# Kernel tuning notes

Hardware: AMD Instinct MI355X
Metric: run time of the kernel (lower is better)

The kernel has to match this reference:

```python
import jax, jax.numpy as jnp
import numpy as np
from jax import lax

DIM = 384
HEADS = 8
DIM_HEAD = 64
INNER = HEADS * DIM_HEAD  # 512
K = 3
B, H, W = 8, 56, 56
EPS = 1e-5
SCALE = DIM_HEAD ** -0.5


def _dw_proj(x, w_dw, bn_g, bn_b, bn_m, bn_v, w_pw):
    """DepthWiseConv2d: depthwise kxk conv (groups=C_in) -> BatchNorm (inference) -> 1x1 conv."""
    c_in = x.shape[1]
    y = lax.conv_general_dilated(
        x, w_dw, window_strides=(1, 1), padding='SAME',
        feature_group_count=c_in,
        dimension_numbers=('NCHW', 'OIHW', 'NCHW'))
    inv = bn_g / jnp.sqrt(bn_v + EPS)
    y = y * inv[None, :, None, None] + (bn_b - bn_m * inv)[None, :, None, None]
    # 1x1 conv as einsum over channels
    return jnp.einsum('bchw,oc->bohw', y, w_pw)


def _split_heads(t):
    # b (h d) x y -> (b h) (x y) d
    b, _, hh, ww = t.shape
    t = t.reshape(b, HEADS, DIM_HEAD, hh * ww)
    return t.transpose(0, 1, 3, 2).reshape(b * HEADS, hh * ww, DIM_HEAD)


def setup_inputs() -> dict:
    key = jax.random.key(0)
    ks = jax.random.split(key, 12)
    inp = {
        'x': jax.random.normal(ks[0], (B, DIM, H, W), jnp.float32),
        'wq_dw': jax.random.normal(ks[1], (DIM, 1, K, K), jnp.float32) * 0.1,
        'wq_bn_g': jax.random.normal(ks[2], (DIM,), jnp.float32) * 0.1 + 1.0,
        'wq_bn_b': jax.random.normal(ks[3], (DIM,), jnp.float32) * 0.1,
        'wq_bn_m': jax.random.normal(ks[4], (DIM,), jnp.float32) * 0.1,
        'wq_bn_v': jax.random.uniform(ks[5], (DIM,), jnp.float32, 0.5, 1.5),
        'wq_pw': jax.random.normal(ks[6], (INNER, DIM), jnp.float32) * (DIM ** -0.5),
        'wkv_dw': jax.random.normal(ks[7], (DIM, 1, K, K), jnp.float32) * 0.1,
        'wkv_bn_g': jax.random.normal(ks[8], (DIM,), jnp.float32) * 0.1 + 1.0,
        'wkv_bn_b': jax.random.normal(ks[9], (DIM,), jnp.float32) * 0.1,
        'wkv_bn_m': jax.random.normal(ks[10], (DIM,), jnp.float32) * 0.1,
        'wkv_bn_v': jax.random.uniform(ks[11], (DIM,), jnp.float32, 0.5, 1.5),
    }
    k2 = jax.random.split(jax.random.fold_in(key, 1), 3)
    inp['wkv_pw'] = jax.random.normal(k2[0], (2 * INNER, DIM), jnp.float32) * (DIM ** -0.5)
    inp['wo'] = jax.random.normal(k2[1], (DIM, INNER), jnp.float32) * (INNER ** -0.5)
    inp['bo'] = jax.random.normal(k2[2], (DIM,), jnp.float32) * 0.01
    return inp


def reference(x, wq_dw, wq_bn_g, wq_bn_b, wq_bn_m, wq_bn_v, wq_pw,
              wkv_dw, wkv_bn_g, wkv_bn_b, wkv_bn_m, wkv_bn_v, wkv_pw, wo, bo):
    b, _, hh, ww = x.shape
    q = _dw_proj(x, wq_dw, wq_bn_g, wq_bn_b, wq_bn_m, wq_bn_v, wq_pw)
    kv = _dw_proj(x, wkv_dw, wkv_bn_g, wkv_bn_b, wkv_bn_m, wkv_bn_v, wkv_pw)
    k, v = kv[:, :INNER], kv[:, INNER:]
    q, k, v = _split_heads(q), _split_heads(k), _split_heads(v)  # (b*h, N, d)

    # Original math: M0 = diag((q*k).sum(-1))*s; M1+M2 = s*q@k^T;
    # out = M0.sum()*v + (M1 - M0)@v + M2@v = M0.sum()*v + s*q@(k^T@v) - diag*v
    diag = (q * k).sum(-1) * SCALE              # (bh, N)
    m0_sum = diag.sum()                          # global scalar
    ktv = jnp.einsum('bnd,bne->bde', k, v)       # (bh, d, d) -- O(N d^2)
    out = m0_sum * v + SCALE * jnp.einsum('bnd,bde->bne', q, ktv) - diag[..., None] * v

    # (b h) (x y) d -> b (h d) x y
    out = out.reshape(b, HEADS, hh * ww, DIM_HEAD).transpose(0, 1, 3, 2)
    out = out.reshape(b, INNER, hh, ww)
    # to_out: 1x1 conv with bias (dropout p=0)
    return jnp.einsum('bchw,oc->bohw', out, wo) + bo[None, :, None, None]
```

## Files before the change

kernel.cpp:

```cpp
#include <hip/hip_runtime.h>

typedef unsigned short u16;

#define N_SP   3136
#define BNCOL  25088
#define NDIM   384
#define NINNER 512
#define SCALE_F 0.125f

typedef __attribute__((ext_vector_type(8))) short bf16x8;
typedef __attribute__((ext_vector_type(4))) float f32x4;

#define AS1 __attribute__((address_space(1)))
#define AS3 __attribute__((address_space(3)))

__device__ __forceinline__ float bf2f(u16 u) {
  union { unsigned int i; float f; } v; v.i = ((unsigned int)u) << 16; return v.f;
}
__device__ __forceinline__ u16 f2bf(float f) {
  union { float f; unsigned int i; } v; v.f = f;
  unsigned int r = v.i + 0x7fffu + ((v.i >> 16) & 1u);
  return (u16)(r >> 16);
}

__device__ __forceinline__ void g2l16(const u16* g, u16* l) {
  __builtin_amdgcn_global_load_lds((const AS1 unsigned int*)g,
                                   (AS3 unsigned int*)l, 16, 0, 0);
}

__global__ __launch_bounds__(256) void cvt_kernel(
    const float* __restrict__ a, const float* __restrict__ b, const float* __restrict__ c,
    u16* __restrict__ oa, u16* __restrict__ ob, u16* __restrict__ oc,
    const float* __restrict__ qdw, const float* __restrict__ qg, const float* __restrict__ qb2,
    const float* __restrict__ qm,  const float* __restrict__ qv,
    const float* __restrict__ kdw, const float* __restrict__ kg, const float* __restrict__ kb2,
    const float* __restrict__ km,  const float* __restrict__ kvv,
    float* __restrict__ fused)
{
  int i = blockIdx.x * 256 + threadIdx.x;
  if (i < 196608) oa[i] = f2bf(a[i]);
  ob[i] = f2bf(b[i]);
  if (i < 196608) oc[i] = f2bf(c[i]);
  if (i < NDIM) {
    float invq = qg[i] * rsqrtf(qv[i] + 1e-5f);
    float invk = kg[i] * rsqrtf(kvv[i] + 1e-5f);
    float* f = fused + i * 20;
#pragma unroll
    for (int j = 0; j < 9; ++j) { f[j] = qdw[i*9+j] * invq; f[10+j] = kdw[i*9+j] * invk; }
    f[9]  = qb2[i] - qm[i] * invq;
    f[19] = kb2[i] - km[i] * invk;
  }
}

__global__ __launch_bounds__(256) void dwbn_kernel(
    const float* __restrict__ x, const float* __restrict__ fused,
    u16* __restrict__ yq, u16* __restrict__ ykv)
{
  __shared__ u16 Lq[64][40];
  __shared__ u16 Lk[64][40];
  int tid = threadIdx.x;
  int bb = blockIdx.z, c0 = blockIdx.y * 32, p0 = blockIdx.x * 64;
  int pl = tid & 63;
  int cg = __builtin_amdgcn_readfirstlane(tid >> 6);
  int p = p0 + pl;
  int h = p / 56, w = p - h * 56;
  int roff[3], coff[3];
  float mr[3], mc[3];
#pragma unroll
  for (int d = 0; d < 3; ++d) {
    int r = h + d - 1;
    bool vr = (r >= 0) && (r < 56);
    roff[d] = (vr ? r : h) * 56;
    mr[d] = vr ? 1.f : 0.f;
    int cc = w + d - 1;
    bool vc = (cc >= 0) && (cc < 56);
    coff[d] = vc ? cc : w;
    mc[d] = vc ? 1.f : 0.f;
  }
  float m9[9];
#pragma unroll
  for (int dh = 0; dh < 3; ++dh)
#pragma unroll
    for (int dw = 0; dw < 3; ++dw) m9[dh*3+dw] = mr[dh] * mc[dw];

  __attribute__((aligned(16))) u16 oq[8], ok[8];
#pragma unroll
  for (int i = 0; i < 8; ++i) {
    int c = c0 + cg * 8 + i;
    const float* xp = x + ((size_t)bb * NDIM + c) * N_SP;
    const float* f = fused + c * 20;
    float v[9];
#pragma unroll
    for (int dh = 0; dh < 3; ++dh)
#pragma unroll
      for (int dw = 0; dw < 3; ++dw)
        v[dh*3+dw] = xp[roff[dh] + coff[dw]];
    float sq = f[9], sk = f[19];
#pragma unroll
    for (int j = 0; j < 9; ++j) {
      float xm = v[j] * m9[j];
      sq += xm * f[j];
      sk += xm * f[10+j];
    }
    oq[i] = f2bf(sq); ok[i] = f2bf(sk);
  }
  *(ushort4*)&Lq[pl][cg * 8]     = *(ushort4*)&oq[0];
  *(ushort4*)&Lq[pl][cg * 8 + 4] = *(ushort4*)&oq[4];
  *(ushort4*)&Lk[pl][cg * 8]     = *(ushort4*)&ok[0];
  *(ushort4*)&Lk[pl][cg * 8 + 4] = *(ushort4*)&ok[4];
  __syncthreads();
  int pr = tid >> 2, cc2 = (tid & 3) * 8;
  size_t g = ((size_t)bb * N_SP + p0 + pr) * NDIM + c0 + cc2;
  *(ushort4*)(yq + g)      = *(ushort4*)&Lq[pr][cc2];
  *(ushort4*)(yq + g + 4)  = *(ushort4*)&Lq[pr][cc2 + 4];
  *(ushort4*)(ykv + g)     = *(ushort4*)&Lk[pr][cc2];
  *(ushort4*)(ykv + g + 4) = *(ushort4*)&Lk[pr][cc2 + 4];
}

__global__ __launch_bounds__(256) void mfma_gemm(
    const u16* __restrict__ A, const u16* __restrict__ B, int Kd,
    u16* __restrict__ Cout, int Cstride,
    int mode, const float* __restrict__ bias, float* __restrict__ Out, int Mt, int Nt)
{
  __shared__ union {
    struct { u16 A[128 * 32]; u16 B[128 * 32]; } s;
    u16 T[64 * 132];
  } lds;
  int bid = blockIdx.x, mt, nt;
  if (Nt == 8) { nt = bid & 7; mt = bid >> 3; }
  else {
    int r = bid & 7, g = bid >> 3;
    mt = g % Mt; nt = (g / Mt) * 8 + r;
    if (nt >= Nt) return;
  }
  int m0 = mt * 128, n0 = nt * 128;

  int tid = threadIdx.x;
  int lane = tid & 63, wv = tid >> 6;
  int wm = (wv >> 1) * 64, wn = (wv & 1) * 64;
  int srow = lane >> 2;
  int sch = (lane & 3) * 8;
  int arow0 = wv * 32;
  const u16* Ag = A + (size_t)(m0 + arow0 + srow) * Kd + sch;
  const u16* Bg = B + (size_t)(n0 + arow0 + srow) * Kd + sch;
  u16* Al = &lds.s.A[arow0 * 32];
  u16* Bl = &lds.s.B[arow0 * 32];
  f32x4 acc[4][4];
#pragma unroll
  for (int i = 0; i < 4; ++i)
#pragma unroll
    for (int j = 0; j < 4; ++j) acc[i][j] = (f32x4){0.f, 0.f, 0.f, 0.f};

  int ml = lane & 15, q8 = (lane >> 4) * 8;
  for (int k0 = 0; k0 < Kd; k0 += 32) {
    g2l16(Ag + k0, Al);
    g2l16(Ag + k0 + (size_t)16 * Kd, Al + 16 * 32);
    g2l16(Bg + k0, Bl);
    g2l16(Bg + k0 + (size_t)16 * Kd, Bl + 16 * 32);
    __syncthreads();
    bf16x8 af[4], bfr[4];
#pragma unroll
    for (int i = 0; i < 4; ++i) {
      af[i]  = *(const bf16x8*)&lds.s.A[(wm + i * 16 + ml) * 32 + q8];
      bfr[i] = *(const bf16x8*)&lds.s.B[(wn + i * 16 + ml) * 32 + q8];
    }
#pragma unroll
    for (int i = 0; i < 4; ++i)
#pragma unroll
      for (int j = 0; j < 4; ++j)
        acc[i][j] = __builtin_amdgcn_mfma_f32_16x16x32_bf16(af[i], bfr[j], acc[i][j], 0, 0, 0);
    __syncthreads();
  }

  if (mode == 0) {
    int q4 = (lane >> 4) * 4;
#pragma unroll
    for (int ph = 0; ph < 2; ++ph) {
      if (ph) __syncthreads();
      if ((wv & 1) == ph) {
#pragma unroll
        for (int i = 0; i < 4; ++i)
#pragma unroll
          for (int j = 0; j < 4; ++j) {
            int nl = j * 16 + ml;
            int m = wm + i * 16 + q4;
            ushort4 o;
            o.x = f2bf(acc[i][j][0]); o.y = f2bf(acc[i][j][1]);
            o.z = f2bf(acc[i][j][2]); o.w = f2bf(acc[i][j][3]);
            *(ushort4*)&lds.T[nl * 132 + m] = o;
          }
      }
      __syncthreads();
#pragma unroll
      for (int it = 0; it < 4; ++it) {
        int nl = it * 16 + (tid >> 4);
        int mc = (tid & 15) * 8;
        ushort4 a = *(ushort4*)&lds.T[nl * 132 + mc];
        ushort4 b = *(ushort4*)&lds.T[nl * 132 + mc + 4];
        u16* gp = Cout + (size_t)(n0 + ph * 64 + nl) * Cstride + m0 + mc;
        *(ushort4*)gp = a;
        *(ushort4*)(gp + 4) = b;
      }
    }
  } else {
    int q4 = (lane >> 4) * 4;
#pragma unroll
    for (int i = 0; i < 4; ++i)
#pragma unroll
      for (int j = 0; j < 4; ++j) {
        int n = n0 + wn + j * 16 + ml;
        int bb = n / N_SP, p = n - bb * N_SP;
#pragma unroll
        for (int rr = 0; rr < 4; ++rr) {
          int m = m0 + wm + i * 16 + q4 + rr;
          Out[((size_t)bb * NDIM + m) * N_SP + p] = acc[i][j][rr] + bias[m];
        }
      }
  }
}

__global__ __launch_bounds__(256) void diag_kernel(
    const u16* __restrict__ Q, const u16* __restrict__ KV,
    float* __restrict__ dg, float* __restrict__ m0)
{
  int hh = blockIdx.y;
  int bn = blockIdx.x * 256 + threadIdx.x;
  const u16* qrow = Q + (size_t)bn * NINNER + hh * 64;
  const u16* kcol = KV + (size_t)(hh * 64) * BNCOL + bn;
  float s = 0.f;
#pragma unroll
  for (int d0 = 0; d0 < 64; d0 += 8) {
    ushort4 a = *(const ushort4*)(qrow + d0);
    ushort4 b = *(const ushort4*)(qrow + d0 + 4);
    const u16* kp = kcol + (size_t)d0 * BNCOL;
    s += bf2f(a.x) * bf2f(kp[0]);
    s += bf2f(a.y) * bf2f(kp[(size_t)1 * BNCOL]);
    s += bf2f(a.z) * bf2f(kp[(size_t)2 * BNCOL]);
    s += bf2f(a.w) * bf2f(kp[(size_t)3 * BNCOL]);
    s += bf2f(b.x) * bf2f(kp[(size_t)4 * BNCOL]);
    s += bf2f(b.y) * bf2f(kp[(size_t)5 * BNCOL]);
    s += bf2f(b.z) * bf2f(kp[(size_t)6 * BNCOL]);
    s += bf2f(b.w) * bf2f(kp[(size_t)7 * BNCOL]);
  }
  s *= SCALE_F;
  dg[(size_t)bn * 8 + hh] = s;
  float r = s;
#pragma unroll
  for (int off = 32; off > 0; off >>= 1) r += __shfl_down(r, off);
  __shared__ float wsum[4];
  if ((threadIdx.x & 63) == 0) wsum[threadIdx.x >> 6] = r;
  __syncthreads();
  if (threadIdx.x == 0) atomicAdd(m0, wsum[0] + wsum[1] + wsum[2] + wsum[3]);
}

__global__ __launch_bounds__(256) void ktv_kernel(
    const u16* __restrict__ KV, float* __restrict__ ktv)
{
  int bh = blockIdx.y, bb = bh >> 3, hh = bh & 7;
  int tid = threadIdx.x;
  int w = tid >> 6, lane = tid & 63;
  int ml = lane & 15, quad = lane >> 4, q8 = quad * 8;
  size_t colbase = (size_t)bb * N_SP + blockIdx.x * 224 + q8;
  const u16* Ar = KV + (size_t)(hh * 64 + w * 16 + ml) * BNCOL + colbase;
  const u16* Br = KV + (size_t)(NINNER + hh * 64 + ml) * BNCOL + colbase;
  f32x4 acc[4];
#pragma unroll
  for (int j = 0; j < 4; ++j) acc[j] = (f32x4){0.f, 0.f, 0.f, 0.f};
#pragma unroll
  for (int t = 0; t < 7; ++t) {
    int po = t * 32;
    bf16x8 a = *(const bf16x8*)(Ar + po);
#pragma unroll
    for (int j = 0; j < 4; ++j) {
      bf16x8 b = *(const bf16x8*)(Br + (size_t)j * 16 * BNCOL + po);
      acc[j] = __builtin_amdgcn_mfma_f32_16x16x32_bf16(a, b, acc[j], 0, 0, 0);
    }
  }
  float* kt = ktv + bh * 4096;
#pragma unroll
  for (int j = 0; j < 4; ++j)
#pragma unroll
    for (int r = 0; r < 4; ++r)
      atomicAdd(&kt[(w * 16 + quad * 4 + r) * 64 + j * 16 + ml], acc[j][r]);
}

__global__ __launch_bounds__(256) void attn_out_kernel(
    const u16* __restrict__ Q, const u16* __restrict__ KV,
    const float* __restrict__ dg, const float* __restrict__ ktv,
    const float* __restrict__ m0p, u16* __restrict__ OutA)
{
  __shared__ u16 Bt[64][72];
  __shared__ u16 T2[64][72];
  __shared__ float ds2[64];
  int bh = blockIdx.y, bb = bh >> 3, hh = bh & 7;
  int p0 = blockIdx.x * 64;
  int tid = threadIdx.x;
  const float* kt = ktv + bh * 4096;
  for (int l = tid; l < 4096; l += 256) {
    int d = l >> 6, e = l & 63;
    Bt[e][d] = f2bf(kt[l]);
  }
  if (tid < 64) ds2[tid] = dg[(size_t)(bb * N_SP + p0 + tid) * 8 + hh];
  __syncthreads();
  int w = tid >> 6, lane = tid & 63;
  int ml = lane & 15, quad = lane >> 4, q8 = quad * 8;
  const u16* Ar = Q + ((size_t)bb * N_SP + p0 + w * 16 + ml) * NINNER + hh * 64 + q8;
  bf16x8 a0 = *(const bf16x8*)Ar;
  bf16x8 a1 = *(const bf16x8*)(Ar + 32);
  f32x4 acc[4];
#pragma unroll
  for (int j = 0; j < 4; ++j) acc[j] = (f32x4){0.f, 0.f, 0.f, 0.f};
#pragma unroll
  for (int j = 0; j < 4; ++j) {
    bf16x8 b0 = *(const bf16x8*)&Bt[j * 16 + ml][q8];
    bf16x8 b1 = *(const bf16x8*)&Bt[j * 16 + ml][32 + q8];
    acc[j] = __builtin_amdgcn_mfma_f32_16x16x32_bf16(a0, b0, acc[j], 0, 0, 0);
    acc[j] = __builtin_amdgcn_mfma_f32_16x16x32_bf16(a1, b1, acc[j], 0, 0, 0);
  }
  float m0v = *m0p;
  size_t pcol = (size_t)bb * N_SP + p0 + w * 16 + quad * 4;
#pragma unroll
  for (int j = 0; j < 4; ++j) {
    const u16* vr = KV + (size_t)(NINNER + hh * 64 + j * 16 + ml) * BNCOL + pcol;
    ushort4 vv = *(const ushort4*)vr;
    const u16* vp = (const u16*)&vv;
#pragma unroll
    for (int r = 0; r < 4; ++r) {
      float dvm = m0v - ds2[w * 16 + quad * 4 + r];
      float o = SCALE_F * acc[j][r] + dvm * bf2f(vp[r]);
      T2[w * 16 + quad * 4 + r][j * 16 + ml] = f2bf(o);
    }
  }
  __syncthreads();
  int pl = tid >> 2, ec = (tid & 3) * 16;
  u16* gp = OutA + ((size_t)bb * N_SP + p0 + pl) * NINNER + hh * 64 + ec;
  *(ushort4*)gp        = *(ushort4*)&T2[pl][ec];
  *(ushort4*)(gp + 4)  = *(ushort4*)&T2[pl][ec + 4];
  *(ushort4*)(gp + 8)  = *(ushort4*)&T2[pl][ec + 8];
  *(ushort4*)(gp + 12) = *(ushort4*)&T2[pl][ec + 12];
}

extern "C" void kernel_launch(void* const* d_in, const int* in_sizes, int n_in,
                              void* d_out, int out_size, void* d_ws, size_t ws_size,
                              hipStream_t stream)
{
  (void)in_sizes; (void)n_in; (void)out_size; (void)ws_size;
  const float* x      = (const float*)d_in[0];
  const float* wq_dw  = (const float*)d_in[1];
  const float* wq_g   = (const float*)d_in[2];
  const float* wq_b   = (const float*)d_in[3];
  const float* wq_m   = (const float*)d_in[4];
  const float* wq_v   = (const float*)d_in[5];
  const float* wq_pw  = (const float*)d_in[6];
  const float* wkv_dw = (const float*)d_in[7];
  const float* wkv_g  = (const float*)d_in[8];
  const float* wkv_b  = (const float*)d_in[9];
  const float* wkv_m  = (const float*)d_in[10];
  const float* wkv_v  = (const float*)d_in[11];
  const float* wkv_pw = (const float*)d_in[12];
  const float* wo     = (const float*)d_in[13];
  const float* bo     = (const float*)d_in[14];
  float* out = (float*)d_out;

  char* ws = (char*)d_ws;
  size_t off = 0;
  auto alloc = [&](size_t bytes) {
    void* p = ws + off; off = (off + bytes + 255) & ~(size_t)255; return p;
  };
  u16* yq   = (u16*)alloc((size_t)BNCOL * NDIM * 2);
  u16* ykv  = (u16*)alloc((size_t)BNCOL * NDIM * 2);
  u16* Qb   = (u16*)alloc((size_t)BNCOL * NINNER * 2);
  u16* KVb  = (u16*)alloc((size_t)2 * NINNER * BNCOL * 2);
  float* dgb  = (float*)alloc((size_t)BNCOL * 8 * 4);
  float* ktvb = (float*)alloc((size_t)64 * 4096 * 4 + 64);
  u16* Wq  = (u16*)alloc((size_t)NINNER * NDIM * 2);
  u16* Wkv = (u16*)alloc((size_t)2 * NINNER * NDIM * 2);
  u16* Wo  = (u16*)alloc((size_t)NDIM * NINNER * 2);
  float* fused = (float*)alloc((size_t)NDIM * 20 * 4);
  float* m0 = ktvb + 64 * 4096;
  u16* OutA = yq;

  hipMemsetAsync(ktvb, 0, (size_t)64 * 4096 * 4 + 4, stream);

  cvt_kernel<<<1536, 256, 0, stream>>>(wq_pw, wkv_pw, wo, Wq, Wkv, Wo,
                                       wq_dw, wq_g, wq_b, wq_m, wq_v,
                                       wkv_dw, wkv_g, wkv_b, wkv_m, wkv_v, fused);

  dwbn_kernel<<<dim3(49, 12, 8), 256, 0, stream>>>(x, fused, yq, ykv);

  mfma_gemm<<<dim3(4 * 200), 256, 0, stream>>>(Wq, yq, NDIM, Qb, NINNER, 0, nullptr, nullptr, 4, 196);
  mfma_gemm<<<dim3(196 * 8), 256, 0, stream>>>(ykv, Wkv, NDIM, KVb, BNCOL, 0, nullptr, nullptr, 196, 8);

  diag_kernel<<<dim3(98, 8), 256, 0, stream>>>(Qb, KVb, dgb, m0);
  ktv_kernel<<<dim3(14, 64), 256, 0, stream>>>(KVb, ktvb);
  attn_out_kernel<<<dim3(49, 64), 256, 0, stream>>>(Qb, KVb, dgb, ktvb, m0, OutA);

  mfma_gemm<<<dim3(3 * 200), 256, 0, stream>>>(Wo, OutA, NINNER, nullptr, 0, 1, bo, out, 3, 196);
}
```

Before: 296.9 us.

## Merge Q and KV projections into one GEMM with channel-major QKV layout

Interleaves the depthwise outputs into a single 768-wide activation buffer and concatenates the Q and KV pointwise weights, so one GEMM launch computes Q, K and V. All three are stored channel-major (d x BNCOL) and written straight from registers, dropping the LDS transpose epilogue. The diag, ktv and attention-output kernels are adapted to the new layout, with K^T V stored transposed and Q gathered with strided loads. The goal is fewer launches and better wave fill. The costs are uncoalesced 2-byte scattered stores in the GEMM epilogue and strided scalar Q loads in attn_out.

```diff
diff --git a/kernel.cpp b/kernel.cpp
--- a/kernel.cpp
+++ b/kernel.cpp
@@ -30,7 +30,7 @@
 
 __global__ __launch_bounds__(256) void cvt_kernel(
     const float* __restrict__ a, const float* __restrict__ b, const float* __restrict__ c,
-    u16* __restrict__ oa, u16* __restrict__ ob, u16* __restrict__ oc,
+    u16* __restrict__ wqkv, u16* __restrict__ wo_o,
     const float* __restrict__ qdw, const float* __restrict__ qg, const float* __restrict__ qb2,
     const float* __restrict__ qm,  const float* __restrict__ qv,
     const float* __restrict__ kdw, const float* __restrict__ kg, const float* __restrict__ kb2,
@@ -38,9 +38,9 @@
     float* __restrict__ fused)
 {
   int i = blockIdx.x * 256 + threadIdx.x;
-  if (i < 196608) oa[i] = f2bf(a[i]);
-  ob[i] = f2bf(b[i]);
-  if (i < 196608) oc[i] = f2bf(c[i]);
+  if (i < 196608) wqkv[i] = f2bf(a[i]);
+  wqkv[196608 + i] = f2bf(b[i]);
+  if (i < 196608) wo_o[i] = f2bf(c[i]);
   if (i < NDIM) {
     float invq = qg[i] * rsqrtf(qv[i] + 1e-5f);
     float invk = kg[i] * rsqrtf(kvv[i] + 1e-5f);
@@ -54,7 +54,7 @@
 
 __global__ __launch_bounds__(256) void dwbn_kernel(
     const float* __restrict__ x, const float* __restrict__ fused,
-    u16* __restrict__ yq, u16* __restrict__ ykv)
+    u16* __restrict__ yact)
 {
   __shared__ u16 Lq[64][40];
   __shared__ u16 Lk[64][40];
@@ -110,30 +110,27 @@
   *(ushort4*)&Lk[pl][cg * 8 + 4] = *(ushort4*)&ok[4];
   __syncthreads();
   int pr = tid >> 2, cc2 = (tid & 3) * 8;
-  size_t g = ((size_t)bb * N_SP + p0 + pr) * NDIM + c0 + cc2;
-  *(ushort4*)(yq + g)      = *(ushort4*)&Lq[pr][cc2];
-  *(ushort4*)(yq + g + 4)  = *(ushort4*)&Lq[pr][cc2 + 4];
-  *(ushort4*)(ykv + g)     = *(ushort4*)&Lk[pr][cc2];
-  *(ushort4*)(ykv + g + 4) = *(ushort4*)&Lk[pr][cc2 + 4];
+  size_t g = ((size_t)bb * N_SP + p0 + pr) * 768 + c0 + cc2;
+  *(ushort4*)(yact + g)            = *(ushort4*)&Lq[pr][cc2];
+  *(ushort4*)(yact + g + 4)        = *(ushort4*)&Lq[pr][cc2 + 4];
+  *(ushort4*)(yact + g + 384)      = *(ushort4*)&Lk[pr][cc2];
+  *(ushort4*)(yact + g + 388)      = *(ushort4*)&Lk[pr][cc2 + 4];
 }
 
 __global__ __launch_bounds__(256) void mfma_gemm(
-    const u16* __restrict__ A, const u16* __restrict__ B, int Kd,
-    u16* __restrict__ Cout, int Cstride,
-    int mode, const float* __restrict__ bias, float* __restrict__ Out, int Mt, int Nt)
-{
-  __shared__ union {
-    struct { u16 A[128 * 32]; u16 B[128 * 32]; } s;
-    u16 T[64 * 132];
-  } lds;
-  int bid = blockIdx.x, mt, nt;
-  if (Nt == 8) { nt = bid & 7; mt = bid >> 3; }
-  else {
-    int r = bid & 7, g = bid >> 3;
-    mt = g % Mt; nt = (g / Mt) * 8 + r;
-    if (nt >= Nt) return;
-  }
+    const u16* __restrict__ A, const u16* __restrict__ B,
+    u16* __restrict__ D, const float* __restrict__ bias, float* __restrict__ Out,
+    int Kd, int bstride, int Mt, int mode)
+{
+  __shared__ u16 As[128 * 32];
+  __shared__ u16 Bs[128 * 32];
+  int bid = blockIdx.x;
+  int x = bid & 7, ii = bid >> 3;
+  int nl = ii / Mt, mt = ii - nl * Mt;
+  int nt = nl * 8 + x;
+  if (nt >= 196) return;
   int m0 = mt * 128, n0 = nt * 128;
+  int koff = (mode == 0 && mt >= 4) ? 384 : 0;
 
   int tid = threadIdx.x;
   int lane = tid & 63, wv = tid >> 6;
@@ -142,9 +139,9 @@
   int sch = (lane & 3) * 8;
   int arow0 = wv * 32;
   const u16* Ag = A + (size_t)(m0 + arow0 + srow) * Kd + sch;
-  const u16* Bg = B + (size_t)(n0 + arow0 + srow) * Kd + sch;
-  u16* Al = &lds.s.A[arow0 * 32];
-  u16* Bl = &lds.s.B[arow0 * 32];
+  const u16* Bg = B + (size_t)(n0 + arow0 + srow) * bstride + koff + sch;
+  u16* Al = &As[arow0 * 32];
+  u16* Bl = &Bs[arow0 * 32];
   f32x4 acc[4][4];
 #pragma unroll
   for (int i = 0; i < 4; ++i)
@@ -156,13 +153,13 @@
     g2l16(Ag + k0, Al);
     g2l16(Ag + k0 + (size_t)16 * Kd, Al + 16 * 32);
     g2l16(Bg + k0, Bl);
-    g2l16(Bg + k0 + (size_t)16 * Kd, Bl + 16 * 32);
+    g2l16(Bg + k0 + (size_t)16 * bstride, Bl + 16 * 32);
     __syncthreads();
     bf16x8 af[4], bfr[4];
 #pragma unroll
     for (int i = 0; i < 4; ++i) {
-      af[i]  = *(const bf16x8*)&lds.s.A[(wm + i * 16 + ml) * 32 + q8];
-      bfr[i] = *(const bf16x8*)&lds.s.B[(wn + i * 16 + ml) * 32 + q8];
+      af[i]  = *(const bf16x8*)&As[(wm + i * 16 + ml) * 32 + q8];
+      bfr[i] = *(const bf16x8*)&Bs[(wn + i * 16 + ml) * 32 + q8];
     }
 #pragma unroll
     for (int i = 0; i < 4; ++i)
@@ -172,38 +169,18 @@
     __syncthreads();
   }
 
+  int q4 = (lane >> 4) * 4;
   if (mode == 0) {
-    int q4 = (lane >> 4) * 4;
-#pragma unroll
-    for (int ph = 0; ph < 2; ++ph) {
-      if (ph) __syncthreads();
-      if ((wv & 1) == ph) {
-#pragma unroll
-        for (int i = 0; i < 4; ++i)
-#pragma unroll
-          for (int j = 0; j < 4; ++j) {
-            int nl = j * 16 + ml;
-            int m = wm + i * 16 + q4;
-            ushort4 o;
-            o.x = f2bf(acc[i][j][0]); o.y = f2bf(acc[i][j][1]);
-            o.z = f2bf(acc[i][j][2]); o.w = f2bf(acc[i][j][3]);
-            *(ushort4*)&lds.T[nl * 132 + m] = o;
-          }
+#pragma unroll
+    for (int i = 0; i < 4; ++i)
+#pragma unroll
+      for (int j = 0; j < 4; ++j) {
+        size_t base = (size_t)(m0 + wm + i * 16 + q4) * BNCOL + n0 + wn + j * 16 + ml;
+#pragma unroll
+        for (int r = 0; r < 4; ++r)
+          D[base + (size_t)r * BNCOL] = f2bf(acc[i][j][r]);
       }
-      __syncthreads();
-#pragma unroll
-      for (int it = 0; it < 4; ++it) {
-        int nl = it * 16 + (tid >> 4);
-        int mc = (tid & 15) * 8;
-        ushort4 a = *(ushort4*)&lds.T[nl * 132 + mc];
-        ushort4 b = *(ushort4*)&lds.T[nl * 132 + mc + 4];
-        u16* gp = Cout + (size_t)(n0 + ph * 64 + nl) * Cstride + m0 + mc;
-        *(ushort4*)gp = a;
-        *(ushort4*)(gp + 4) = b;
-      }
-    }
   } else {
-    int q4 = (lane >> 4) * 4;
 #pragma unroll
     for (int i = 0; i < 4; ++i)
 #pragma unroll
@@ -211,39 +188,27 @@
         int n = n0 + wn + j * 16 + ml;
         int bb = n / N_SP, p = n - bb * N_SP;
 #pragma unroll
-        for (int rr = 0; rr < 4; ++rr) {
-          int m = m0 + wm + i * 16 + q4 + rr;
-          Out[((size_t)bb * NDIM + m) * N_SP + p] = acc[i][j][rr] + bias[m];
+        for (int r = 0; r < 4; ++r) {
+          int m = m0 + wm + i * 16 + q4 + r;
+          Out[((size_t)bb * NDIM + m) * N_SP + p] = acc[i][j][r] + bias[m];
         }
       }
   }
 }
 
 __global__ __launch_bounds__(256) void diag_kernel(
-    const u16* __restrict__ Q, const u16* __restrict__ KV,
-    float* __restrict__ dg, float* __restrict__ m0)
+    const u16* __restrict__ QKV, float* __restrict__ dg, float* __restrict__ m0)
 {
   int hh = blockIdx.y;
   int bn = blockIdx.x * 256 + threadIdx.x;
-  const u16* qrow = Q + (size_t)bn * NINNER + hh * 64;
-  const u16* kcol = KV + (size_t)(hh * 64) * BNCOL + bn;
+  const u16* qp = QKV + (size_t)(hh * 64) * BNCOL + bn;
+  const u16* kp = QKV + (size_t)(512 + hh * 64) * BNCOL + bn;
   float s = 0.f;
-#pragma unroll
-  for (int d0 = 0; d0 < 64; d0 += 8) {
-    ushort4 a = *(const ushort4*)(qrow + d0);
-    ushort4 b = *(const ushort4*)(qrow + d0 + 4);
-    const u16* kp = kcol + (size_t)d0 * BNCOL;
-    s += bf2f(a.x) * bf2f(kp[0]);
-    s += bf2f(a.y) * bf2f(kp[(size_t)1 * BNCOL]);
-    s += bf2f(a.z) * bf2f(kp[(size_t)2 * BNCOL]);
-    s += bf2f(a.w) * bf2f(kp[(size_t)3 * BNCOL]);
-    s += bf2f(b.x) * bf2f(kp[(size_t)4 * BNCOL]);
-    s += bf2f(b.y) * bf2f(kp[(size_t)5 * BNCOL]);
-    s += bf2f(b.z) * bf2f(kp[(size_t)6 * BNCOL]);
-    s += bf2f(b.w) * bf2f(kp[(size_t)7 * BNCOL]);
-  }
+#pragma unroll 8
+  for (int d = 0; d < 64; ++d)
+    s += bf2f(qp[(size_t)d * BNCOL]) * bf2f(kp[(size_t)d * BNCOL]);
   s *= SCALE_F;
-  dg[(size_t)bn * 8 + hh] = s;
+  dg[(size_t)hh * BNCOL + bn] = s;
   float r = s;
 #pragma unroll
   for (int off = 32; off > 0; off >>= 1) r += __shfl_down(r, off);
@@ -254,15 +219,15 @@
 }
 
 __global__ __launch_bounds__(256) void ktv_kernel(
-    const u16* __restrict__ KV, float* __restrict__ ktv)
+    const u16* __restrict__ QKV, float* __restrict__ ktv)
 {
   int bh = blockIdx.y, bb = bh >> 3, hh = bh & 7;
   int tid = threadIdx.x;
   int w = tid >> 6, lane = tid & 63;
   int ml = lane & 15, quad = lane >> 4, q8 = quad * 8;
   size_t colbase = (size_t)bb * N_SP + blockIdx.x * 224 + q8;
-  const u16* Ar = KV + (size_t)(hh * 64 + w * 16 + ml) * BNCOL + colbase;
-  const u16* Br = KV + (size_t)(NINNER + hh * 64 + ml) * BNCOL + colbase;
+  const u16* Ar = QKV + (size_t)(512 + hh * 64 + w * 16 + ml) * BNCOL + colbase;
+  const u16* Br = QKV + (size_t)(1024 + hh * 64 + ml) * BNCOL + colbase;
   f32x4 acc[4];
 #pragma unroll
   for (int j = 0; j < 4; ++j) acc[j] = (f32x4){0.f, 0.f, 0.f, 0.f};
@@ -281,59 +246,59 @@
   for (int j = 0; j < 4; ++j)
 #pragma unroll
     for (int r = 0; r < 4; ++r)
-      atomicAdd(&kt[(w * 16 + quad * 4 + r) * 64 + j * 16 + ml], acc[j][r]);
+      atomicAdd(&kt[(j * 16 + ml) * 64 + w * 16 + quad * 4 + r], acc[j][r]);
 }
 
 __global__ __launch_bounds__(256) void attn_out_kernel(
-    const u16* __restrict__ Q, const u16* __restrict__ KV,
-    const float* __restrict__ dg, const float* __restrict__ ktv,
-    const float* __restrict__ m0p, u16* __restrict__ OutA)
-{
-  __shared__ u16 Bt[64][72];
+    const u16* __restrict__ QKV, const float* __restrict__ dg,
+    const float* __restrict__ ktv, const float* __restrict__ m0p,
+    u16* __restrict__ OutA)
+{
+  __shared__ u16 Kt[64][72];
   __shared__ u16 T2[64][72];
   __shared__ float ds2[64];
   int bh = blockIdx.y, bb = bh >> 3, hh = bh & 7;
   int p0 = blockIdx.x * 64;
   int tid = threadIdx.x;
   const float* kt = ktv + bh * 4096;
-  for (int l = tid; l < 4096; l += 256) {
-    int d = l >> 6, e = l & 63;
-    Bt[e][d] = f2bf(kt[l]);
-  }
-  if (tid < 64) ds2[tid] = dg[(size_t)(bb * N_SP + p0 + tid) * 8 + hh];
+  for (int l = tid; l < 4096; l += 256) Kt[l >> 6][l & 63] = f2bf(kt[l]);
+  size_t pb = (size_t)bb * N_SP + p0;
+  if (tid < 64) ds2[tid] = dg[(size_t)hh * BNCOL + pb + tid];
   __syncthreads();
   int w = tid >> 6, lane = tid & 63;
   int ml = lane & 15, quad = lane >> 4, q8 = quad * 8;
-  const u16* Ar = Q + ((size_t)bb * N_SP + p0 + w * 16 + ml) * NINNER + hh * 64 + q8;
-  bf16x8 a0 = *(const bf16x8*)Ar;
-  bf16x8 a1 = *(const bf16x8*)(Ar + 32);
+  bf16x8 a0 = *(const bf16x8*)&Kt[w * 16 + ml][q8];
+  bf16x8 a1 = *(const bf16x8*)&Kt[w * 16 + ml][32 + q8];
+  const u16* Qbase = QKV + (size_t)(hh * 64 + q8) * BNCOL + pb + ml;
   f32x4 acc[4];
 #pragma unroll
   for (int j = 0; j < 4; ++j) acc[j] = (f32x4){0.f, 0.f, 0.f, 0.f};
 #pragma unroll
   for (int j = 0; j < 4; ++j) {
-    bf16x8 b0 = *(const bf16x8*)&Bt[j * 16 + ml][q8];
-    bf16x8 b1 = *(const bf16x8*)&Bt[j * 16 + ml][32 + q8];
+    bf16x8 b0, b1;
+#pragma unroll
+    for (int jj = 0; jj < 8; ++jj) {
+      b0[jj] = (short)Qbase[(size_t)jj * BNCOL + j * 16];
+      b1[jj] = (short)Qbase[(size_t)(32 + jj) * BNCOL + j * 16];
+    }
     acc[j] = __builtin_amdgcn_mfma_f32_16x16x32_bf16(a0, b0, acc[j], 0, 0, 0);
     acc[j] = __builtin_amdgcn_mfma_f32_16x16x32_bf16(a1, b1, acc[j], 0, 0, 0);
   }
   float m0v = *m0p;
-  size_t pcol = (size_t)bb * N_SP + p0 + w * 16 + quad * 4;
 #pragma unroll
   for (int j = 0; j < 4; ++j) {
-    const u16* vr = KV + (size_t)(NINNER + hh * 64 + j * 16 + ml) * BNCOL + pcol;
-    ushort4 vv = *(const ushort4*)vr;
-    const u16* vp = (const u16*)&vv;
+    int pcol = j * 16 + ml;
+    float dvm = m0v - ds2[pcol];
+    const u16* vr = QKV + (size_t)(1024 + hh * 64 + w * 16 + quad * 4) * BNCOL + pb + pcol;
 #pragma unroll
     for (int r = 0; r < 4; ++r) {
-      float dvm = m0v - ds2[w * 16 + quad * 4 + r];
-      float o = SCALE_F * acc[j][r] + dvm * bf2f(vp[r]);
-      T2[w * 16 + quad * 4 + r][j * 16 + ml] = f2bf(o);
+      float o = SCALE_F * acc[j][r] + dvm * bf2f(vr[(size_t)r * BNCOL]);
+      T2[pcol][w * 16 + quad * 4 + r] = f2bf(o);
     }
   }
   __syncthreads();
   int pl = tid >> 2, ec = (tid & 3) * 16;
-  u16* gp = OutA + ((size_t)bb * N_SP + p0 + pl) * NINNER + hh * 64 + ec;
+  u16* gp = OutA + (pb + pl) * NINNER + hh * 64 + ec;
   *(ushort4*)gp        = *(ushort4*)&T2[pl][ec];
   *(ushort4*)(gp + 4)  = *(ushort4*)&T2[pl][ec + 4];
   *(ushort4*)(gp + 8)  = *(ushort4*)&T2[pl][ec + 8];
@@ -367,33 +332,31 @@
   auto alloc = [&](size_t bytes) {
     void* p = ws + off; off = (off + bytes + 255) & ~(size_t)255; return p;
   };
-  u16* yq   = (u16*)alloc((size_t)BNCOL * NDIM * 2);
-  u16* ykv  = (u16*)alloc((size_t)BNCOL * NDIM * 2);
-  u16* Qb   = (u16*)alloc((size_t)BNCOL * NINNER * 2);
-  u16* KVb  = (u16*)alloc((size_t)2 * NINNER * BNCOL * 2);
-  float* dgb  = (float*)alloc((size_t)BNCOL * 8 * 4);
+  u16* Yact  = (u16*)alloc((size_t)BNCOL * 768 * 2);
+  u16* QKVb  = (u16*)alloc((size_t)1536 * BNCOL * 2);
+  float* dgb  = (float*)alloc((size_t)8 * BNCOL * 4);
   float* ktvb = (float*)alloc((size_t)64 * 4096 * 4 + 64);
-  u16* Wq  = (u16*)alloc((size_t)NINNER * NDIM * 2);
-  u16* Wkv = (u16*)alloc((size_t)2 * NINNER * NDIM * 2);
-  u16* Wo  = (u16*)alloc((size_t)NDIM * NINNER * 2);
+  u16* Wqkv = (u16*)alloc((size_t)1536 * NDIM * 2);
+  u16* Wo   = (u16*)alloc((size_t)NDIM * NINNER * 2);
   float* fused = (float*)alloc((size_t)NDIM * 20 * 4);
   float* m0 = ktvb + 64 * 4096;
-  u16* OutA = yq;
+  u16* OutA = Yact;
 
   hipMemsetAsync(ktvb, 0, (size_t)64 * 4096 * 4 + 4, stream);
 
-  cvt_kernel<<<1536, 256, 0, stream>>>(wq_pw, wkv_pw, wo, Wq, Wkv, Wo,
+  cvt_kernel<<<1536, 256, 0, stream>>>(wq_pw, wkv_pw, wo, Wqkv, Wo,
                                        wq_dw, wq_g, wq_b, wq_m, wq_v,
                                        wkv_dw, wkv_g, wkv_b, wkv_m, wkv_v, fused);
 
-  dwbn_kernel<<<dim3(49, 12, 8), 256, 0, stream>>>(x, fused, yq, ykv);
-
-  mfma_gemm<<<dim3(4 * 200), 256, 0, stream>>>(Wq, yq, NDIM, Qb, NINNER, 0, nullptr, nullptr, 4, 196);
-  mfma_gemm<<<dim3(196 * 8), 256, 0, stream>>>(ykv, Wkv, NDIM, KVb, BNCOL, 0, nullptr, nullptr, 196, 8);
-
-  diag_kernel<<<dim3(98, 8), 256, 0, stream>>>(Qb, KVb, dgb, m0);
-  ktv_kernel<<<dim3(14, 64), 256, 0, stream>>>(KVb, ktvb);
-  attn_out_kernel<<<dim3(49, 64), 256, 0, stream>>>(Qb, KVb, dgb, ktvb, m0, OutA);
-
-  mfma_gemm<<<dim3(3 * 200), 256, 0, stream>>>(Wo, OutA, NINNER, nullptr, 0, 1, bo, out, 3, 196);
-}
+  dwbn_kernel<<<dim3(49, 12, 8), 256, 0, stream>>>(x, fused, Yact);
+
+  mfma_gemm<<<dim3(8 * 25 * 12), 256, 0, stream>>>(Wqkv, Yact, QKVb, nullptr, nullptr,
+                                                   NDIM, 768, 12, 0);
+
+  diag_kernel<<<dim3(98, 8), 256, 0, stream>>>(QKVb, dgb, m0);
+  ktv_kernel<<<dim3(14, 64), 256, 0, stream>>>(QKVb, ktvb);
+  attn_out_kernel<<<dim3(49, 64), 256, 0, stream>>>(QKVb, dgb, ktvb, m0, OutA);
+
+  mfma_gemm<<<dim3(8 * 25 * 3), 256, 0, stream>>>(Wo, OutA, nullptr, bo, out,
+                                                  NINNER, NINNER, 3, 1);
+}
```

Result: slower. 326.0 us (+9.8%).
